# Optimization experiments

Hardware: AMD Instinct MI355X
Metric: run time of the kernel (lower is better)

The kernel has to match this reference:

```python
import jax, jax.numpy as jnp
import numpy as np

B, S, D, H = 32, 512, 1024, 16
DH = D // H
EPS = 1e-5
NEG = -1e9


def layer_norm(x, g, b):
    mu = jnp.mean(x, axis=-1, keepdims=True)
    var = jnp.mean(jnp.square(x - mu), axis=-1, keepdims=True)
    return (x - mu) * jax.lax.rsqrt(var + EPS) * g + b


def setup_inputs() -> dict:
    key = jax.random.key(0)
    ks = jax.random.split(key, 12)
    s = 1.0 / np.sqrt(D)
    inp = {
        "qk": jax.random.normal(ks[0], (B, S, D), jnp.float32),
        "v": jax.random.normal(ks[1], (B, S, D), jnp.float32),
        "mask": jax.random.randint(ks[2], (B, S), 0, 2).astype(jnp.int32),
        "qk_ln_g": jnp.ones((D,), jnp.float32),
        "qk_ln_b": jnp.zeros((D,), jnp.float32),
        "v_ln_g": jnp.ones((D,), jnp.float32),
        "v_ln_b": jnp.zeros((D,), jnp.float32),
        "Wq": jax.random.normal(ks[3], (D, D), jnp.float32) * s,
        "bq": jnp.zeros((D,), jnp.float32),
        "Wk": jax.random.normal(ks[4], (D, D), jnp.float32) * s,
        "bk": jnp.zeros((D,), jnp.float32),
        "Wv": jax.random.normal(ks[5], (D, D), jnp.float32) * s,
        "bv": jnp.zeros((D,), jnp.float32),
        "Wo": jax.random.normal(ks[6], (D, D), jnp.float32) * s,
        "bo": jnp.zeros((D,), jnp.float32),
    }
    return inp


def reference(qk, v, mask, qk_ln_g, qk_ln_b, v_ln_g, v_ln_b,
              Wq, bq, Wk, bk, Wv, bv, Wo, bo):
    # dual pre-norm
    qk_n = layer_norm(qk, qk_ln_g, qk_ln_b)          # [B,S,D]
    v_n = layer_norm(v, v_ln_g, v_ln_b)              # [B,S,D]
    # projections -> [B,S,H,DH]
    q = (qk_n @ Wq + bq).reshape(B, S, H, DH)
    k = (qk_n @ Wk + bk).reshape(B, S, H, DH)
    vv = (v_n @ Wv + bv).reshape(B, S, H, DH)
    # attention scores with key-padding mask
    scores = jnp.einsum("bqhd,bkhd->bhqk", q, k) / np.sqrt(DH)
    scores = jnp.where(mask[:, None, None, :] == 0, NEG, scores)
    attn = jax.nn.softmax(scores, axis=-1)           # [B,H,Sq,Sk]
    ctx = jnp.einsum("bhqk,bkhd->bqhd", attn, vv).reshape(B, S, D)
    a = ctx @ Wo + bo                                # output projection
    # residual on the normalized v (dropout is identity at eval)
    return v_n + a
```

## Files before the change

kernel.cpp:

```cpp
#include <hip/hip_runtime.h>
#include <hip/hip_bf16.h>

typedef __bf16 bf16;
typedef __bf16 bf16x2 __attribute__((ext_vector_type(2)));
typedef __bf16 bf16x4 __attribute__((ext_vector_type(4)));
typedef __bf16 bf16x8 __attribute__((ext_vector_type(8)));
typedef float f32x4 __attribute__((ext_vector_type(4)));

#define B_ 32
#define S_ 512
#define D_ 1024
#define H_ 16
#define DH_ 64
#define M_ (B_*S_)

#if __has_builtin(__builtin_amdgcn_exp2f)
#define FEXP2 __builtin_amdgcn_exp2f
#else
#define FEXP2 exp2f
#endif

__device__ __forceinline__ void async16(const void* g, void* l) {
  __builtin_amdgcn_global_load_lds(
      (const __attribute__((address_space(1))) unsigned int*)g,
      (__attribute__((address_space(3))) unsigned int*)l, 16, 0, 0);
}

__global__ __launch_bounds__(256) void ln_bf16(
    const float* __restrict__ qk, const float* __restrict__ v,
    const float* __restrict__ g1, const float* __restrict__ b1,
    const float* __restrict__ g2, const float* __restrict__ b2,
    bf16* __restrict__ o1, bf16* __restrict__ o2)
{
  int row = blockIdx.x;
  const float* src; const float* g; const float* b; bf16* o; int r;
  if (row < M_) { src=qk; g=g1; b=b1; o=o1; r=row; }
  else          { src=v;  g=g2; b=b2; o=o2; r=row-M_; }
  int t = threadIdx.x;
  float4 x = ((const float4*)(src + (size_t)r*D_))[t];
  float s  = x.x+x.y+x.z+x.w;
  float ss = x.x*x.x + x.y*x.y + x.z*x.z + x.w*x.w;
  #pragma unroll
  for (int off=32; off>=1; off>>=1) {
    s  += __shfl_xor(s,  off, 64);
    ss += __shfl_xor(ss, off, 64);
  }
  __shared__ float red[8];
  int w = t>>6, l = t&63;
  if (l==0){ red[w]=s; red[4+w]=ss; }
  __syncthreads();
  s  = red[0]+red[1]+red[2]+red[3];
  ss = red[4]+red[5]+red[6]+red[7];
  float mu  = s*(1.f/D_);
  float var = ss*(1.f/D_) - mu*mu;
  float rs  = rsqrtf(var + 1e-5f);
  float4 gg = ((const float4*)g)[t];
  float4 bb = ((const float4*)b)[t];
  bf16x4 ov;
  ov[0] = (bf16)((x.x-mu)*rs*gg.x + bb.x);
  ov[1] = (bf16)((x.y-mu)*rs*gg.y + bb.y);
  ov[2] = (bf16)((x.z-mu)*rs*gg.z + bb.z);
  ov[3] = (bf16)((x.w-mu)*rs*gg.w + bb.w);
  ((bf16x4*)(o + (size_t)r*D_))[t] = ov;
}

__global__ void wtrans(const float* __restrict__ W0, const float* __restrict__ W1,
                       const float* __restrict__ W2, const float* __restrict__ W3,
                       bf16* __restrict__ o0, bf16* __restrict__ o1,
                       bf16* __restrict__ o2, bf16* __restrict__ o3)
{
  int z = blockIdx.z;
  const float* W = z==0?W0: z==1?W1: z==2?W2: W3;
  bf16* o        = z==0?o0: z==1?o1: z==2?o2: o3;
  __shared__ float tile[32][33];
  int n0 = blockIdx.x*32, k0 = blockIdx.y*32;
  int tx = threadIdx.x, ty = threadIdx.y;
  #pragma unroll
  for (int i=0;i<4;i++) tile[ty + i*8][tx] = W[(size_t)(k0+ty+i*8)*D_ + n0+tx];
  __syncthreads();
  #pragma unroll
  for (int i=0;i<4;i++) o[(size_t)(n0+ty+i*8)*D_ + k0+tx] = (bf16)tile[tx][ty+i*8];
}

template<int MODE>
__global__ __launch_bounds__(256) void gemm_bt(
    const bf16* __restrict__ A, const bf16* __restrict__ Bt,
    const float* __restrict__ bias0, const float* __restrict__ bias1,
    const bf16* __restrict__ res,
    bf16* __restrict__ out0, bf16* __restrict__ out1, float* __restrict__ outf)
{
  __shared__ bf16 A_sh[2][128*64];
  __shared__ bf16 B_sh[2][128*64];
  int t = threadIdx.x;
  int nwg  = gridDim.x * gridDim.y;
  int orig = blockIdx.y * gridDim.x + blockIdx.x;
  int qch  = nwg >> 3;
  int wg   = (orig & 7) * qch + (orig >> 3);
  int bx = wg % gridDim.x, by = wg / gridDim.x;
  int n0 = bx*128, m0 = by*128;
  int w = t>>6, l = t&63, lr = l&15, lg = (l>>4)&3;
  int wm = w>>1, wn = w&1;

  auto stage = [&](int buf, int kt){
    const bf16* Ab = A  + (size_t)m0*D_ + kt*64;
    const bf16* Bb = Bt + (size_t)n0*D_ + kt*64;
    #pragma unroll
    for (int i=0;i<4;i++){
      int c = i*256 + t;
      int row = c>>3, slot = (c&7) ^ (row&7);
      async16(Ab + (size_t)row*D_ + slot*8, &A_sh[buf][c*8]);
      async16(Bb + (size_t)row*D_ + slot*8, &B_sh[buf][c*8]);
    }
  };

  f32x4 acc[4][4];
  #pragma unroll
  for (int m=0;m<4;m++)
    #pragma unroll
    for (int n=0;n<4;n++) acc[m][n] = (f32x4){0.f,0.f,0.f,0.f};

  stage(0, 0);
  stage(1, 1);
  asm volatile("s_waitcnt vmcnt(8)" ::: "memory");
  __builtin_amdgcn_s_barrier();

  for (int kt=0; kt<16; ++kt) {
    int cur = kt & 1;
    bf16x8 af[4][2], bfr[4][2];
    #pragma unroll
    for (int m=0;m<4;m++){
      int row = wm*64 + m*16 + lr;
      #pragma unroll
      for (int kk=0;kk<2;kk++)
        af[m][kk] = *(const bf16x8*)&A_sh[cur][row*64 + (((kk*4+lg)^(lr&7))*8)];
    }
    #pragma unroll
    for (int n=0;n<4;n++){
      int row = wn*64 + n*16 + lr;
      #pragma unroll
      for (int kk=0;kk<2;kk++)
        bfr[n][kk] = *(const bf16x8*)&B_sh[cur][row*64 + (((kk*4+lg)^(lr&7))*8)];
    }
    asm volatile("s_waitcnt lgkmcnt(0)" ::: "memory");
    __builtin_amdgcn_sched_barrier(0);
    __builtin_amdgcn_s_barrier();
    if (kt+2 < 16) stage(cur, kt+2);
    __builtin_amdgcn_s_setprio(1);
    #pragma unroll
    for (int kk=0;kk<2;kk++)
      #pragma unroll
      for (int m=0;m<4;m++)
        #pragma unroll
        for (int n=0;n<4;n++)
          acc[m][n] = __builtin_amdgcn_mfma_f32_16x16x32_bf16(af[m][kk], bfr[n][kk], acc[m][n], 0,0,0);
    __builtin_amdgcn_s_setprio(0);
    if (kt < 14)       asm volatile("s_waitcnt vmcnt(8)" ::: "memory");
    else if (kt == 14) asm volatile("s_waitcnt vmcnt(0)" ::: "memory");
    if (kt < 15) { __builtin_amdgcn_sched_barrier(0); __builtin_amdgcn_s_barrier(); }
  }

  if (MODE == 0) {
    #pragma unroll
    for (int n=0;n<4;n++){
      int col = n0 + wn*64 + n*16 + lr;
      bf16* dst; int c;
      if (col < D_) { dst = out0; c = col; } else { dst = out1; c = col - D_; }
      float bv = (col < D_) ? bias0[c] : bias1[c];
      #pragma unroll
      for (int m=0;m<4;m++){
        #pragma unroll
        for (int j=0;j<4;j++){
          size_t row = (size_t)m0 + wm*64 + m*16 + lg*4 + j;
          dst[row*D_ + c] = (bf16)(acc[m][n][j] + bv);
        }
      }
    }
  } else if (MODE == 1) {
    #pragma unroll
    for (int n=0;n<4;n++){
      int col = n0 + wn*64 + n*16 + lr;
      int h = col >> 6, dh = col & 63;
      float bv = bias0[col];
      #pragma unroll
      for (int m=0;m<4;m++){
        int row = m0 + wm*64 + m*16 + lg*4;
        int b = row >> 9, s = row & 511;
        bf16x4 pk;
        #pragma unroll
        for (int j=0;j<4;j++) pk[j] = (bf16)(acc[m][n][j] + bv);
        *(bf16x4*)&out0[((size_t)(b*H_ + h)*DH_ + dh)*S_ + s] = pk;
      }
    }
  } else {
    #pragma unroll
    for (int m=0;m<4;m++){
      #pragma unroll
      for (int j=0;j<4;j++){
        size_t row = (size_t)m0 + wm*64 + m*16 + lg*4 + j;
        #pragma unroll
        for (int n=0;n<4;n++){
          int col = n0 + wn*64 + n*16 + lr;
          size_t idx = row*D_ + col;
          outf[idx] = acc[m][n][j] + bias0[col] + (float)res[idx];
        }
      }
    }
  }
}

__global__ __launch_bounds__(512) void attn_fwd(
    const bf16* __restrict__ Q, const bf16* __restrict__ K,
    const bf16* __restrict__ VT, const int* __restrict__ mask,
    bf16* __restrict__ ctx)
{
  int flat = blockIdx.x + (blockIdx.y<<1) + (blockIdx.z<<5);
  int work = (flat & 7)*128 + (flat >> 3);
  int qt = work & 1, h = (work>>1) & 15, b = work >> 5;
  int q0 = qt*256;
  int t = threadIdx.x, w = t>>6, l = t&63, lr = l&15, lg = (l>>4)&3;

  __shared__ bf16 K_s[2][4096];
  __shared__ bf16 V_s[2][4096];
  __shared__ float msk[512];

  const float SC = 0.125f * 1.44269504f;
  msk[t] = mask[b*S_+t] ? 0.f : -1.44269504e9f;

  size_t qbase  = ((size_t)(b*S_ + q0)*H_ + h)*DH_;
  size_t vtbase = (size_t)(b*H_ + h)*DH_*S_;

  auto stageKV = [&](int slot, int kt){
    size_t kb = ((size_t)(b*S_ + kt*64)*H_ + h)*DH_;
    size_t vb = vtbase + kt*64;
    int clr=t&15, clg=(t>>4)&3, ckk=(t>>6)&1, n16=t>>7;
    async16(K + kb + (size_t)(n16*16+clr)*D_ + ckk*32 + clg*8, &K_s[slot][t*8]);
    async16(VT + vb + (size_t)(n16*16+clr)*S_ + ckk*32 + clg*8, &V_s[slot][t*8]);
  };

  bf16x8 qa[2][2];
  #pragma unroll
  for (int s=0;s<2;s++)
    #pragma unroll
    for (int kk=0;kk<2;kk++)
      qa[s][kk] = *(const bf16x8*)(Q + qbase + (size_t)(w*32 + s*16 + lr)*D_ + kk*32 + lg*8);

  stageKV(0, 0);
  stageKV(1, 1);
  asm volatile("s_waitcnt vmcnt(2) lgkmcnt(0)" ::: "memory");
  __builtin_amdgcn_s_barrier();

  f32x4 cacc[2][4];
  #pragma unroll
  for (int s=0;s<2;s++)
    #pragma unroll
    for (int n=0;n<4;n++) cacc[s][n] = (f32x4){0.f,0.f,0.f,0.f};
  float mrun[2] = {-3.0e38f, -3.0e38f};
  float lrun[2] = {0.f, 0.f};

  union UPA { unsigned u[4]; bf16x8 v; };
  UPA pa[2][2];

  for (int kt=0; kt<8; ++kt) {
    int cur = kt & 1;
    const bf16* Ks = K_s[cur];
    const bf16* Vs = V_s[cur];

    bf16x8 kf[4][2];
    #pragma unroll
    for (int n=0;n<4;n++)
      #pragma unroll
      for (int kk=0;kk<2;kk++)
        kf[n][kk] = *(const bf16x8*)&Ks[(((n*2+kk)*4+lg)*16+lr)*8];

    #pragma unroll
    for (int s=0;s<2;s++){
      float p[4][4];
      #pragma unroll
      for (int n=0;n<4;n++){
        f32x4 sa = (f32x4){0.f,0.f,0.f,0.f};
        #pragma unroll
        for (int kk=0;kk<2;kk++)
          sa = __builtin_amdgcn_mfma_f32_16x16x32_bf16(kf[n][kk], qa[s][kk], sa, 0,0,0);
        float4 mk = *(const float4*)&msk[kt*64 + n*16 + lg*4];
        p[n][0] = sa[0]*SC + mk.x;
        p[n][1] = sa[1]*SC + mk.y;
        p[n][2] = sa[2]*SC + mk.z;
        p[n][3] = sa[3]*SC + mk.w;
      }

      float pm = fmaxf(fmaxf(p[0][0],p[0][1]),fmaxf(p[0][2],p[0][3]));
      #pragma unroll
      for (int n=1;n<4;n++)
        pm = fmaxf(pm, fmaxf(fmaxf(p[n][0],p[n][1]),fmaxf(p[n][2],p[n][3])));
      pm = fmaxf(pm, __shfl_xor(pm, 16, 64));
      pm = fmaxf(pm, __shfl_xor(pm, 32, 64));

      if (__any((int)(pm - mrun[s] > 8.f))) {
        float mnew  = fmaxf(mrun[s], pm);
        float alpha = FEXP2(mrun[s] - mnew);
        mrun[s] = mnew;
        lrun[s] *= alpha;
        #pragma unroll
        for (int n=0;n<4;n++) cacc[s][n] *= alpha;
      }
      float ps = 0.f;
      #pragma unroll
      for (int n=0;n<4;n++)
        #pragma unroll
        for (int j=0;j<4;j++){ p[n][j] = FEXP2(p[n][j] - mrun[s]); ps += p[n][j]; }
      ps += __shfl_xor(ps, 16, 64);
      ps += __shfl_xor(ps, 32, 64);
      lrun[s] += ps;

      unsigned pk[4][2];
      #pragma unroll
      for (int n=0;n<4;n++)
        #pragma unroll
        for (int i=0;i<2;i++){
          union { bf16x2 v; unsigned u; } u2;
          u2.v[0] = (bf16)p[n][2*i];
          u2.v[1] = (bf16)p[n][2*i+1];
          pk[n][i] = u2.u;
        }
      int srcbase = (l&15) + ((l&16)<<1);
      #pragma unroll
      for (int w4=0; w4<4; ++w4){
        int src = srcbase + ((w4&2)<<3);
        unsigned lo0 = __shfl(pk[0][w4&1], src, 64);
        unsigned hi0 = __shfl(pk[1][w4&1], src, 64);
        unsigned lo1 = __shfl(pk[2][w4&1], src, 64);
        unsigned hi1 = __shfl(pk[3][w4&1], src, 64);
        pa[s][0].u[w4] = (l&32) ? hi0 : lo0;
        pa[s][1].u[w4] = (l&32) ? hi1 : lo1;
      }
    }

    __builtin_amdgcn_s_setprio(1);
    #pragma unroll
    for (int nd=0;nd<4;nd++){
      bf16x8 vb0 = *(const bf16x8*)&Vs[(((nd*2+0)*4+lg)*16+lr)*8];
      bf16x8 vb1 = *(const bf16x8*)&Vs[(((nd*2+1)*4+lg)*16+lr)*8];
      #pragma unroll
      for (int s=0;s<2;s++){
        cacc[s][nd] = __builtin_amdgcn_mfma_f32_16x16x32_bf16(vb0, pa[s][0].v, cacc[s][nd], 0,0,0);
        cacc[s][nd] = __builtin_amdgcn_mfma_f32_16x16x32_bf16(vb1, pa[s][1].v, cacc[s][nd], 0,0,0);
      }
    }
    __builtin_amdgcn_s_setprio(0);

    asm volatile("s_waitcnt lgkmcnt(0)" ::: "memory");
    __builtin_amdgcn_sched_barrier(0);
    __builtin_amdgcn_s_barrier();
    if (kt+2 < 8) stageKV(cur, kt+2);

    if (kt < 6)       asm volatile("s_waitcnt vmcnt(2)" ::: "memory");
    else if (kt == 6) asm volatile("s_waitcnt vmcnt(0)" ::: "memory");
    if (kt < 7) { __builtin_amdgcn_sched_barrier(0); __builtin_amdgcn_s_barrier(); }
  }

  #pragma unroll
  for (int s=0;s<2;s++){
    float rl = 1.0f / lrun[s];
    size_t obase = qbase + (size_t)(w*32 + s*16 + lr)*D_;
    #pragma unroll
    for (int nd=0;nd<4;nd++){
      bf16x4 o4;
      #pragma unroll
      for (int j=0;j<4;j++) o4[j] = (bf16)(cacc[s][nd][j]*rl);
      *(bf16x4*)&ctx[obase + nd*16 + lg*4] = o4;
    }
  }
}

extern "C" void kernel_launch(void* const* d_in, const int* in_sizes, int n_in,
                              void* d_out, int out_size, void* d_ws, size_t ws_size,
                              hipStream_t stream)
{
  (void)in_sizes; (void)n_in; (void)out_size; (void)ws_size;
  const float* qk   = (const float*)d_in[0];
  const float* v    = (const float*)d_in[1];
  const int*   mask = (const int*)  d_in[2];
  const float* qk_g = (const float*)d_in[3];
  const float* qk_b = (const float*)d_in[4];
  const float* v_g  = (const float*)d_in[5];
  const float* v_b  = (const float*)d_in[6];
  const float* Wq   = (const float*)d_in[7];
  const float* bq   = (const float*)d_in[8];
  const float* Wk   = (const float*)d_in[9];
  const float* bk   = (const float*)d_in[10];
  const float* Wv   = (const float*)d_in[11];
  const float* bv   = (const float*)d_in[12];
  const float* Wo   = (const float*)d_in[13];
  const float* bo   = (const float*)d_in[14];
  float* out = (float*)d_out;

  char* ws = (char*)d_ws;
  size_t off = 0;
  auto alloc = [&](size_t bytes){ void* p = ws + off; off += (bytes + 255) & ~(size_t)255; return p; };
  bf16* qkn  = (bf16*)alloc((size_t)M_*D_*2);
  bf16* vn   = (bf16*)alloc((size_t)M_*D_*2);
  bf16* Qb   = (bf16*)alloc((size_t)M_*D_*2);
  bf16* Kb   = (bf16*)alloc((size_t)M_*D_*2);
  bf16* VTb  = (bf16*)alloc((size_t)M_*D_*2);
  bf16* Cb   = (bf16*)alloc((size_t)M_*D_*2);
  bf16* WqkT = (bf16*)alloc((size_t)2*D_*D_*2);
  bf16* WvT  = (bf16*)alloc((size_t)D_*D_*2);
  bf16* WoT  = (bf16*)alloc((size_t)D_*D_*2);

  ln_bf16<<<2*M_, 256, 0, stream>>>(qk, v, qk_g, qk_b, v_g, v_b, qkn, vn);
  wtrans<<<dim3(32,32,4), dim3(32,8), 0, stream>>>(Wq, Wk, Wv, Wo,
      WqkT, WqkT + (size_t)D_*D_, WvT, WoT);
  gemm_bt<0><<<dim3(16,128), 256, 0, stream>>>(qkn, WqkT, bq, bk, nullptr, Qb, Kb, nullptr);
  gemm_bt<1><<<dim3(8,128),  256, 0, stream>>>(vn,  WvT,  bv, nullptr, nullptr, VTb, nullptr, nullptr);
  attn_fwd<<<dim3(2, 16, 32), 512, 0, stream>>>(Qb, Kb, VTb, mask, Cb);
  gemm_bt<2><<<dim3(8,128),  256, 0, stream>>>(Cb, WoT, bo, nullptr, vn, nullptr, nullptr, out);
}
```

Before: 272.8 us.

## Double attention key tile to 128 and halve pipeline iterations

The attention kernel now stages 128-key K/V tiles per iteration instead of 64, which halves the loop count and the barrier/sync overhead per key and amortizes softmax rescale checks over more keys. The LDS buffers double in size, the V staging layout is changed to match the wider tile, and launch bounds request 4 blocks per CU. The risks are higher register pressure from the larger score arrays and lower occupancy from the larger LDS footprint.

```diff
diff --git a/kernel.cpp b/kernel.cpp
--- a/kernel.cpp
+++ b/kernel.cpp
@@ -208,7 +208,7 @@
   }
 }
 
-__global__ __launch_bounds__(512) void attn_fwd(
+__global__ __launch_bounds__(512, 4) void attn_fwd(
     const bf16* __restrict__ Q, const bf16* __restrict__ K,
     const bf16* __restrict__ VT, const int* __restrict__ mask,
     bf16* __restrict__ ctx)
@@ -219,8 +219,8 @@
   int q0 = qt*256;
   int t = threadIdx.x, w = t>>6, l = t&63, lr = l&15, lg = (l>>4)&3;
 
-  __shared__ bf16 K_s[2][4096];
-  __shared__ bf16 V_s[2][4096];
+  __shared__ bf16 K_s[2][8192];
+  __shared__ bf16 V_s[2][8192];
   __shared__ float msk[512];
 
   const float SC = 0.125f * 1.44269504f;
@@ -229,12 +229,18 @@
   size_t qbase  = ((size_t)(b*S_ + q0)*H_ + h)*DH_;
   size_t vtbase = (size_t)(b*H_ + h)*DH_*S_;
 
-  auto stageKV = [&](int slot, int kt){
-    size_t kb = ((size_t)(b*S_ + kt*64)*H_ + h)*DH_;
-    size_t vb = vtbase + kt*64;
-    int clr=t&15, clg=(t>>4)&3, ckk=(t>>6)&1, n16=t>>7;
-    async16(K + kb + (size_t)(n16*16+clr)*D_ + ckk*32 + clg*8, &K_s[slot][t*8]);
-    async16(VT + vb + (size_t)(n16*16+clr)*S_ + ckk*32 + clg*8, &V_s[slot][t*8]);
+  auto stageKV = [&](int slot, int kt2){
+    size_t kb = ((size_t)(b*S_ + kt2*128)*H_ + h)*DH_;
+    size_t vb = vtbase + kt2*128;
+    #pragma unroll
+    for (int i=0;i<2;i++){
+      int c = i*512 + t;
+      int clr = c&15, clg = (c>>4)&3;
+      int kkk = (c>>6)&1, kn16 = c>>7;
+      int vkk = (c>>6)&3, vn16 = (c>>8)&3;
+      async16(K + kb + (size_t)(kn16*16+clr)*D_ + kkk*32 + clg*8, &K_s[slot][c*8]);
+      async16(VT + vb + (size_t)(vn16*16+clr)*S_ + vkk*32 + clg*8, &V_s[slot][c*8]);
+    }
   };
 
   bf16x8 qa[2][2];
@@ -246,7 +252,7 @@
 
   stageKV(0, 0);
   stageKV(1, 1);
-  asm volatile("s_waitcnt vmcnt(2) lgkmcnt(0)" ::: "memory");
+  asm volatile("s_waitcnt vmcnt(4) lgkmcnt(0)" ::: "memory");
   __builtin_amdgcn_s_barrier();
 
   f32x4 cacc[2][4];
@@ -258,30 +264,25 @@
   float lrun[2] = {0.f, 0.f};
 
   union UPA { unsigned u[4]; bf16x8 v; };
-  UPA pa[2][2];
-
-  for (int kt=0; kt<8; ++kt) {
-    int cur = kt & 1;
+  UPA pa[2][4];
+
+  for (int kt2=0; kt2<4; ++kt2) {
+    int cur = kt2 & 1;
     const bf16* Ks = K_s[cur];
     const bf16* Vs = V_s[cur];
 
-    bf16x8 kf[4][2];
-    #pragma unroll
-    for (int n=0;n<4;n++)
-      #pragma unroll
-      for (int kk=0;kk<2;kk++)
-        kf[n][kk] = *(const bf16x8*)&Ks[(((n*2+kk)*4+lg)*16+lr)*8];
-
     #pragma unroll
     for (int s=0;s<2;s++){
-      float p[4][4];
-      #pragma unroll
-      for (int n=0;n<4;n++){
+      float p[8][4];
+      #pragma unroll
+      for (int n=0;n<8;n++){
         f32x4 sa = (f32x4){0.f,0.f,0.f,0.f};
         #pragma unroll
-        for (int kk=0;kk<2;kk++)
-          sa = __builtin_amdgcn_mfma_f32_16x16x32_bf16(kf[n][kk], qa[s][kk], sa, 0,0,0);
-        float4 mk = *(const float4*)&msk[kt*64 + n*16 + lg*4];
+        for (int kk=0;kk<2;kk++){
+          bf16x8 kf = *(const bf16x8*)&Ks[(((n*2+kk)*4+lg)*16+lr)*8];
+          sa = __builtin_amdgcn_mfma_f32_16x16x32_bf16(kf, qa[s][kk], sa, 0,0,0);
+        }
+        float4 mk = *(const float4*)&msk[kt2*128 + n*16 + lg*4];
         p[n][0] = sa[0]*SC + mk.x;
         p[n][1] = sa[1]*SC + mk.y;
         p[n][2] = sa[2]*SC + mk.z;
@@ -290,7 +291,7 @@
 
       float pm = fmaxf(fmaxf(p[0][0],p[0][1]),fmaxf(p[0][2],p[0][3]));
       #pragma unroll
-      for (int n=1;n<4;n++)
+      for (int n=1;n<8;n++)
         pm = fmaxf(pm, fmaxf(fmaxf(p[n][0],p[n][1]),fmaxf(p[n][2],p[n][3])));
       pm = fmaxf(pm, __shfl_xor(pm, 16, 64));
       pm = fmaxf(pm, __shfl_xor(pm, 32, 64));
@@ -305,16 +306,16 @@
       }
       float ps = 0.f;
       #pragma unroll
-      for (int n=0;n<4;n++)
+      for (int n=0;n<8;n++)
         #pragma unroll
         for (int j=0;j<4;j++){ p[n][j] = FEXP2(p[n][j] - mrun[s]); ps += p[n][j]; }
       ps += __shfl_xor(ps, 16, 64);
       ps += __shfl_xor(ps, 32, 64);
       lrun[s] += ps;
 
-      unsigned pk[4][2];
-      #pragma unroll
-      for (int n=0;n<4;n++)
+      unsigned pk[8][2];
+      #pragma unroll
+      for (int n=0;n<8;n++)
         #pragma unroll
         for (int i=0;i<2;i++){
           union { bf16x2 v; unsigned u; } u2;
@@ -324,38 +325,36 @@
         }
       int srcbase = (l&15) + ((l&16)<<1);
       #pragma unroll
-      for (int w4=0; w4<4; ++w4){
-        int src = srcbase + ((w4&2)<<3);
-        unsigned lo0 = __shfl(pk[0][w4&1], src, 64);
-        unsigned hi0 = __shfl(pk[1][w4&1], src, 64);
-        unsigned lo1 = __shfl(pk[2][w4&1], src, 64);
-        unsigned hi1 = __shfl(pk[3][w4&1], src, 64);
-        pa[s][0].u[w4] = (l&32) ? hi0 : lo0;
-        pa[s][1].u[w4] = (l&32) ? hi1 : lo1;
+      for (int kk=0;kk<4;kk++){
+        #pragma unroll
+        for (int w4=0; w4<4; ++w4){
+          int src = srcbase + ((w4&2)<<3);
+          unsigned lo = __shfl(pk[2*kk  ][w4&1], src, 64);
+          unsigned hi = __shfl(pk[2*kk+1][w4&1], src, 64);
+          pa[s][kk].u[w4] = (l&32) ? hi : lo;
+        }
       }
     }
 
     __builtin_amdgcn_s_setprio(1);
     #pragma unroll
-    for (int nd=0;nd<4;nd++){
-      bf16x8 vb0 = *(const bf16x8*)&Vs[(((nd*2+0)*4+lg)*16+lr)*8];
-      bf16x8 vb1 = *(const bf16x8*)&Vs[(((nd*2+1)*4+lg)*16+lr)*8];
-      #pragma unroll
-      for (int s=0;s<2;s++){
-        cacc[s][nd] = __builtin_amdgcn_mfma_f32_16x16x32_bf16(vb0, pa[s][0].v, cacc[s][nd], 0,0,0);
-        cacc[s][nd] = __builtin_amdgcn_mfma_f32_16x16x32_bf16(vb1, pa[s][1].v, cacc[s][nd], 0,0,0);
-      }
-    }
+    for (int nd=0;nd<4;nd++)
+      #pragma unroll
+      for (int kk=0;kk<4;kk++){
+        bf16x8 vb = *(const bf16x8*)&Vs[(((nd*4+kk)*4+lg)*16+lr)*8];
+        cacc[0][nd] = __builtin_amdgcn_mfma_f32_16x16x32_bf16(vb, pa[0][kk].v, cacc[0][nd], 0,0,0);
+        cacc[1][nd] = __builtin_amdgcn_mfma_f32_16x16x32_bf16(vb, pa[1][kk].v, cacc[1][nd], 0,0,0);
+      }
     __builtin_amdgcn_s_setprio(0);
 
     asm volatile("s_waitcnt lgkmcnt(0)" ::: "memory");
     __builtin_amdgcn_sched_barrier(0);
     __builtin_amdgcn_s_barrier();
-    if (kt+2 < 8) stageKV(cur, kt+2);
-
-    if (kt < 6)       asm volatile("s_waitcnt vmcnt(2)" ::: "memory");
-    else if (kt == 6) asm volatile("s_waitcnt vmcnt(0)" ::: "memory");
-    if (kt < 7) { __builtin_amdgcn_sched_barrier(0); __builtin_amdgcn_s_barrier(); }
+    if (kt2 < 2) stageKV(cur, kt2+2);
+
+    if (kt2 < 2)       asm volatile("s_waitcnt vmcnt(4)" ::: "memory");
+    else if (kt2 == 2) asm volatile("s_waitcnt vmcnt(0)" ::: "memory");
+    if (kt2 < 3) { __builtin_amdgcn_sched_barrier(0); __builtin_amdgcn_s_barrier(); }
   }
 
   #pragma unroll
```

Result: slower. 312.2 us (+14.4%).

## Pre-swizzle V into MFMA fragment layout to drop P shuffles

Applied to the files above, without the earlier changes.

The V projection epilogue now writes V in a per-tile layout that matches the MFMA operand order the attention kernel uses, so each 64-key tile is one contiguous 8 KB block. The attention kernel loads V with plain contiguous async copies and builds the P operand straight from its registers, which removes the cross-lane shuffles. This works because the key permutation applied to V matches the one implied by P's accumulator layout. The cost is more scattered stores in the GEMM epilogue, and correctness depends on that index mapping being exact.

```diff
diff --git a/kernel.cpp b/kernel.cpp
--- a/kernel.cpp
+++ b/kernel.cpp
@@ -179,16 +179,20 @@
     #pragma unroll
     for (int n=0;n<4;n++){
       int col = n0 + wn*64 + n*16 + lr;
-      int h = col >> 6, dh = col & 63;
+      int hh = col >> 6, dh = col & 63;
+      int nd = dh >> 4, lrk = dh & 15;
       float bv = bias0[col];
       #pragma unroll
       for (int m=0;m<4;m++){
         int row = m0 + wm*64 + m*16 + lg*4;
-        int b = row >> 9, s = row & 511;
-        bf16x4 pk;
-        #pragma unroll
-        for (int j=0;j<4;j++) pk[j] = (bf16)(acc[m][n][j] + bv);
-        *(bf16x4*)&out0[((size_t)(b*H_ + h)*DH_ + dh)*S_ + s] = pk;
+        int bb = row >> 9, sl = row & 511;
+        int kt = sl >> 6, l0 = sl & 63;
+        int kk = (l0>>5)&1, h8 = (l0>>4)&1, lgk = (l0>>2)&3;
+        int c  = ((nd*2+kk)*4+lgk)*16 + lrk;
+        bf16x4 pk4;
+        #pragma unroll
+        for (int j=0;j<4;j++) pk4[j] = (bf16)(acc[m][n][j] + bv);
+        *(bf16x4*)&out0[(size_t)(((bb*H_ + hh)*8 + kt)*4096) + c*8 + h8*4] = pk4;
       }
     }
   } else {
@@ -210,7 +214,7 @@
 
 __global__ __launch_bounds__(512) void attn_fwd(
     const bf16* __restrict__ Q, const bf16* __restrict__ K,
-    const bf16* __restrict__ VT, const int* __restrict__ mask,
+    const bf16* __restrict__ VF, const int* __restrict__ mask,
     bf16* __restrict__ ctx)
 {
   int flat = blockIdx.x + (blockIdx.y<<1) + (blockIdx.z<<5);
@@ -227,14 +231,13 @@
   msk[t] = mask[b*S_+t] ? 0.f : -1.44269504e9f;
 
   size_t qbase  = ((size_t)(b*S_ + q0)*H_ + h)*DH_;
-  size_t vtbase = (size_t)(b*H_ + h)*DH_*S_;
+  size_t vfbase = (size_t)(b*H_ + h)*8*4096;
 
   auto stageKV = [&](int slot, int kt){
     size_t kb = ((size_t)(b*S_ + kt*64)*H_ + h)*DH_;
-    size_t vb = vtbase + kt*64;
     int clr=t&15, clg=(t>>4)&3, ckk=(t>>6)&1, n16=t>>7;
     async16(K + kb + (size_t)(n16*16+clr)*D_ + ckk*32 + clg*8, &K_s[slot][t*8]);
-    async16(VT + vb + (size_t)(n16*16+clr)*S_ + ckk*32 + clg*8, &V_s[slot][t*8]);
+    async16(VF + vfbase + (size_t)kt*4096 + t*8, &V_s[slot][t*8]);
   };
 
   bf16x8 qa[2][2];
@@ -322,16 +325,12 @@
           u2.v[1] = (bf16)p[n][2*i+1];
           pk[n][i] = u2.u;
         }
-      int srcbase = (l&15) + ((l&16)<<1);
-      #pragma unroll
-      for (int w4=0; w4<4; ++w4){
-        int src = srcbase + ((w4&2)<<3);
-        unsigned lo0 = __shfl(pk[0][w4&1], src, 64);
-        unsigned hi0 = __shfl(pk[1][w4&1], src, 64);
-        unsigned lo1 = __shfl(pk[2][w4&1], src, 64);
-        unsigned hi1 = __shfl(pk[3][w4&1], src, 64);
-        pa[s][0].u[w4] = (l&32) ? hi0 : lo0;
-        pa[s][1].u[w4] = (l&32) ? hi1 : lo1;
+      #pragma unroll
+      for (int kk=0;kk<2;kk++){
+        pa[s][kk].u[0] = pk[2*kk  ][0];
+        pa[s][kk].u[1] = pk[2*kk  ][1];
+        pa[s][kk].u[2] = pk[2*kk+1][0];
+        pa[s][kk].u[3] = pk[2*kk+1][1];
       }
     }
 
@@ -401,7 +400,7 @@
   bf16* vn   = (bf16*)alloc((size_t)M_*D_*2);
   bf16* Qb   = (bf16*)alloc((size_t)M_*D_*2);
   bf16* Kb   = (bf16*)alloc((size_t)M_*D_*2);
-  bf16* VTb  = (bf16*)alloc((size_t)M_*D_*2);
+  bf16* VFb  = (bf16*)alloc((size_t)M_*D_*2);
   bf16* Cb   = (bf16*)alloc((size_t)M_*D_*2);
   bf16* WqkT = (bf16*)alloc((size_t)2*D_*D_*2);
   bf16* WvT  = (bf16*)alloc((size_t)D_*D_*2);
@@ -411,7 +410,7 @@
   wtrans<<<dim3(32,32,4), dim3(32,8), 0, stream>>>(Wq, Wk, Wv, Wo,
       WqkT, WqkT + (size_t)D_*D_, WvT, WoT);
   gemm_bt<0><<<dim3(16,128), 256, 0, stream>>>(qkn, WqkT, bq, bk, nullptr, Qb, Kb, nullptr);
-  gemm_bt<1><<<dim3(8,128),  256, 0, stream>>>(vn,  WvT,  bv, nullptr, nullptr, VTb, nullptr, nullptr);
-  attn_fwd<<<dim3(2, 16, 32), 512, 0, stream>>>(Qb, Kb, VTb, mask, Cb);
+  gemm_bt<1><<<dim3(8,128),  256, 0, stream>>>(vn,  WvT,  bv, nullptr, nullptr, VFb, nullptr, nullptr);
+  attn_fwd<<<dim3(2, 16, 32), 512, 0, stream>>>(Qb, Kb, VFb, mask, Cb);
   gemm_bt<2><<<dim3(8,128),  256, 0, stream>>>(Cb, WoT, bo, nullptr, vn, nullptr, nullptr, out);
 }
```

Measured after the change: 257.4 us, median of 3. 5.6% less time.
